# Performance work log

Hardware: AMD Instinct MI355X
Metric: run time of the kernel (lower is better)

The kernel has to match this reference:

```python
import jax, jax.numpy as jnp
import numpy as np

C = 27
SIZE = 448
PATCH = 14
G = PATCH * 4          # target_global = 56
SHN = (SIZE * SIZE) // (PATCH * PATCH)  # split_head_num = 1024
PW, GW = 0.75, 0.25    # patch_weight, global_weight
EPS = 1e-5


def setup_inputs() -> dict:
    key = jax.random.key(0)
    ks = jax.random.split(key, 9)
    s = 0.02
    return {
        "x": jax.random.normal(ks[0], (4, C, SIZE, SIZE), dtype=jnp.float32),
        "gn_w": jnp.ones((C,), jnp.float32),
        "gn_b": jnp.zeros((C,), jnp.float32),
        "q_w": jax.random.normal(ks[1], (C, C), jnp.float32) * s,
        "q_b": jax.random.normal(ks[2], (C,), jnp.float32) * s,
        "k_w": jax.random.normal(ks[3], (C, C), jnp.float32) * s,
        "k_b": jax.random.normal(ks[4], (C,), jnp.float32) * s,
        "v_w": jax.random.normal(ks[5], (C, C), jnp.float32) * s,
        "v_b": jax.random.normal(ks[6], (C,), jnp.float32) * s,
        "proj_w": jax.random.normal(ks[7], (C, C), jnp.float32) * s,
    }


def _conv1x1(w, bias, t):
    out = jnp.einsum('oc,bchw->bohw', w, t)
    return out if bias is None else out + bias[None, :, None, None]


def _bmm_attn(q, k, v, scale):
    # q,k,v: (b, d, n). w = softmax(q^T k * scale, axis=2); h = einsum over keys.
    w = jax.nn.softmax(jnp.einsum('bdn,bdm->bnm', q, k) * scale, axis=2)
    return jnp.einsum('bdj,bij->bdi', v, w)


def reference(x, gn_w, gn_b, q_w, q_b, k_w, k_b, v_w, v_b, proj_w):
    b, c, H, W = x.shape
    # GroupNorm(num_groups=1): normalize over (C,H,W) per sample
    mu = jnp.mean(x, axis=(1, 2, 3), keepdims=True)
    var = jnp.var(x, axis=(1, 2, 3), keepdims=True)
    xn = (x - mu) * jax.lax.rsqrt(var + EPS)
    xn = xn * gn_w[None, :, None, None] + gn_b[None, :, None, None]

    q = _conv1x1(q_w, q_b, xn)
    k = _conv1x1(k_w, k_b, xn)
    v = _conv1x1(v_w, v_b, xn)

    # AdaptiveAvgPool2d 448 -> 56 (exact factor 8): block mean
    f = H // G
    pool = lambda t: t.reshape(b, c, G, f, G, f).mean(axis=(3, 5))

    # patch-wise bmm attention: view (b, c*SHN, PATCH^2), attend over 196 positions
    d = c * SHN
    n = PATCH * PATCH
    qf = q.reshape(b, d, n)
    kf = k.reshape(b, d, n)
    vf = v.reshape(b, d, n)
    h_patch = _bmm_attn(qf, kf, vf, 1.0 / np.sqrt(d).astype(np.float32)).reshape(b, c, H, W)

    # global pooled bmm attention over 56*56 positions with dim c, then nearest upsample
    qg = pool(q).reshape(b, c, G * G)
    kg = pool(k).reshape(b, c, G * G)
    vg = pool(v).reshape(b, c, G * G)
    hg = _bmm_attn(qg, kg, vg, 1.0 / np.sqrt(c).astype(np.float32)).reshape(b, c, G, G)
    hg = jnp.repeat(jnp.repeat(hg, f, axis=2), f, axis=3)  # nearest upsample to (H, W)

    h_in = PW * h_patch + GW * hg
    return x + _conv1x1(proj_w, None, h_in)
```

## Files before the change

kernel.cpp:

```cpp
#include <hip/hip_runtime.h>
#include <hip/hip_bf16.h>
#include <cstdint>

namespace {
constexpr int BB = 4;
constexpr int CC = 27;
constexpr int HW = 448 * 448;
constexpr long long CHW = (long long)CC * HW;
constexpr int NP = 196;
constexpr int GG = 56 * 56;
constexpr int DTOT = CC * 1024;
constexpr float SCALE_P = 0.0060140449f;
constexpr float SCALE_G = 0.1924500897f;
constexpr float EPSV = 1e-5f;
constexpr int KCH = 512;
constexpr int NKS = DTOT / KCH;
constexpr int MPAD = 224;
constexpr int ROWB = 128;
constexpr int WFRAG = 7 * 13 * 64 * 8;
constexpr int XST = 40;
constexpr int GKC = 224;
constexpr int KST = 40;
constexpr int VST = 232;
constexpr int HST = 204;
}

typedef __attribute__((ext_vector_type(8))) short short8;
typedef __attribute__((ext_vector_type(4))) float f32x4;

__device__ __forceinline__ float bf2f(unsigned short u) {
    return __uint_as_float(((uint32_t)u) << 16);
}

__device__ __forceinline__ ushort f2bf(float f) {
    union { __hip_bfloat16 h; ushort u; } cv;
    cv.h = __float2bfloat16(f);
    return cv.u;
}

__global__ void k_fold(const float* __restrict__ pjw, const float* __restrict__ vw,
                       const float* __restrict__ vb, float* __restrict__ pvw,
                       float* __restrict__ pvb) {
    __shared__ float pj[729], vv[729], vbs[27];
    int t = threadIdx.x;
    for (int i = t; i < 729; i += 256) { pj[i] = pjw[i]; vv[i] = vw[i]; }
    if (t < 27) vbs[t] = vb[t];
    __syncthreads();
    for (int i = t; i < 729; i += 256) {
        int o = i / 27, c2 = i - (i / 27) * 27;
        float s = 0.f;
#pragma unroll
        for (int c = 0; c < 27; c++) s += pj[o * 27 + c] * vv[c * 27 + c2];
        pvw[i] = s;
    }
    if (t < 27) {
        float s = 0.f;
#pragma unroll
        for (int c = 0; c < 27; c++) s += pj[t * 27 + c] * vbs[c];
        pvb[t] = s;
    }
}

__global__ void k_gn_partial(const float* __restrict__ x, float* __restrict__ part) {
    int blk = blockIdx.x;
    int b = blk >> 10;
    int chunk = blk & 1023;
    const int CLEN = (int)(CHW / 1024);
    const float* p = x + (size_t)b * CHW + (size_t)chunk * CLEN;
    float s = 0.f, ss = 0.f;
    for (int i = threadIdx.x; i < CLEN; i += 256) {
        float v = p[i];
        s += v; ss += v * v;
    }
    for (int o = 32; o; o >>= 1) { s += __shfl_down(s, o); ss += __shfl_down(ss, o); }
    __shared__ float ls[4], lss[4];
    int wid = threadIdx.x >> 6, lane = threadIdx.x & 63;
    if (lane == 0) { ls[wid] = s; lss[wid] = ss; }
    __syncthreads();
    if (threadIdx.x == 0) {
        float S = ls[0] + ls[1] + ls[2] + ls[3];
        float SS = lss[0] + lss[1] + lss[2] + lss[3];
        part[blk * 2] = S; part[blk * 2 + 1] = SS;
    }
}

__global__ void k_gn_final(const float* __restrict__ part, float* __restrict__ stats) {
    int b = blockIdx.x;
    float s = 0.f, ss = 0.f;
    for (int i = threadIdx.x; i < 1024; i += 256) {
        s += part[(b * 1024 + i) * 2];
        ss += part[(b * 1024 + i) * 2 + 1];
    }
    for (int o = 32; o; o >>= 1) { s += __shfl_down(s, o); ss += __shfl_down(ss, o); }
    __shared__ float ls[4], lss[4];
    int wid = threadIdx.x >> 6, lane = threadIdx.x & 63;
    if (lane == 0) { ls[wid] = s; lss[wid] = ss; }
    __syncthreads();
    if (threadIdx.x == 0) {
        float S = ls[0] + ls[1] + ls[2] + ls[3];
        float SS = lss[0] + lss[1] + lss[2] + lss[3];
        float mean = S / (float)CHW;
        float var = SS / (float)CHW - mean * mean;
        stats[b * 2] = mean;
        stats[b * 2 + 1] = rsqrtf(var + EPSV);
    }
}

__global__ __launch_bounds__(256, 2)
void k_qkv_mfma(const float* __restrict__ x, const float* __restrict__ stats,
                const float* __restrict__ qw, const float* __restrict__ qb,
                const float* __restrict__ kw, const float* __restrict__ kb,
                const float* __restrict__ vw, const float* __restrict__ vb,
                const float* __restrict__ gnw, const float* __restrict__ gnb,
                __hip_bfloat16* __restrict__ qkv) {
    __shared__ ushort xs[256 * XST];
    __shared__ ushort wls[96 * XST];
    __shared__ __align__(16) float bls[96];
    __shared__ float gwls[27], gbls[27];

    int tid = threadIdx.x;
    int P0 = blockIdx.x * 256;
    int b = P0 / HW;
    int hw0 = P0 - b * HW;

    for (int i = tid; i < 96 * 32; i += 256) {
        int row = i >> 5, c = i & 31;
        float wv = 0.f;
        if (c < 27 && row < 81) {
            int t = (row >= 54) ? 2 : (row >= 27 ? 1 : 0);
            int oc = row - t * 27;
            const float* wp = (t == 0) ? qw : (t == 1) ? kw : vw;
            wv = wp[oc * 27 + c];
        }
        wls[row * XST + c] = f2bf(wv);
    }
    if (tid < 96) {
        float bv = 0.f;
        if (tid < 27) bv = qb[tid];
        else if (tid < 54) bv = kb[tid - 27];
        else if (tid < 81) bv = vb[tid - 54];
        bls[tid] = bv;
    }
    if (tid < 27) { gwls[tid] = gnw[tid]; gbls[tid] = gnb[tid]; }
    float mean = stats[b * 2], rstd = stats[b * 2 + 1];
    __syncthreads();

    {
        const float* xp = x + (size_t)b * CHW + hw0 + tid;
        ushort xv[28];
#pragma unroll
        for (int c = 0; c < 27; c++) {
            float v = (xp[(size_t)c * HW] - mean) * rstd * gwls[c] + gbls[c];
            xv[c] = f2bf(v);
        }
        xv[27] = 0;
        uint32_t* xrow = reinterpret_cast<uint32_t*>(&xs[tid * XST]);
#pragma unroll
        for (int i = 0; i < 14; i++)
            xrow[i] = (uint32_t)xv[2 * i] | ((uint32_t)xv[2 * i + 1] << 16);
        xrow[14] = 0; xrow[15] = 0;
    }
    __syncthreads();

    int w = tid >> 6, l = tid & 63;
    int lrow = l & 15, kg = l >> 4;

    short8 afr[6];
    f32x4 binit[6];
#pragma unroll
    for (int mt = 0; mt < 6; mt++) {
        afr[mt] = *reinterpret_cast<const short8*>(&wls[(mt * 16 + lrow) * XST + kg * 8]);
        binit[mt] = *reinterpret_cast<const f32x4*>(&bls[mt * 16 + kg * 4]);
    }

    f32x4 acc[4][6];
#pragma unroll
    for (int pt = 0; pt < 4; pt++) {
        const short8 bfr = *reinterpret_cast<const short8*>(
            &xs[(w * 64 + pt * 16 + lrow) * XST + kg * 8]);
#pragma unroll
        for (int mt = 0; mt < 6; mt++)
            acc[pt][mt] = __builtin_amdgcn_mfma_f32_16x16x32_bf16(afr[mt], bfr, binit[mt], 0, 0, 0);
    }

    ushort* ob = (ushort*)qkv;
#pragma unroll
    for (int pt = 0; pt < 4; pt++) {
        int hw = hw0 + w * 64 + pt * 16 + lrow;
#pragma unroll
        for (int mt = 0; mt < 6; mt++) {
#pragma unroll
            for (int r = 0; r < 4; r++) {
                int o = mt * 16 + kg * 4 + r;
                if (o < 81) {
                    int t = (o >= 54) ? 2 : (o >= 27 ? 1 : 0);
                    int oc = o - t * 27;
                    ob[((size_t)t * BB + b) * CHW + (size_t)oc * HW + hw] = f2bf(acc[pt][mt][r]);
                }
            }
        }
    }
}

__global__ void k_pool(const __hip_bfloat16* __restrict__ src, float* __restrict__ dst) {
    int idx = blockIdx.x * 256 + threadIdx.x;
    int g = idx % GG;
    int t = idx / GG;
    int c = t % 27;
    int b = t / 27;
    int gh = g / 56, gw = g - (g / 56) * 56;
    const ushort* sp = (const ushort*)src + (size_t)(b * 27 + c) * HW + (size_t)(gh * 8) * 448 + gw * 8;
    float s = 0.f;
#pragma unroll
    for (int r = 0; r < 8; r++) {
        const ushort4 a = *reinterpret_cast<const ushort4*>(sp + r * 448);
        const ushort4 d = *reinterpret_cast<const ushort4*>(sp + r * 448 + 4);
        s += bf2f(a.x) + bf2f(a.y) + bf2f(a.z) + bf2f(a.w)
           + bf2f(d.x) + bf2f(d.y) + bf2f(d.z) + bf2f(d.w);
    }
    dst[((size_t)b * GG + g) * 27 + c] = s * (1.f / 64.f);
}

__global__ __launch_bounds__(448, 1)
void k_spart_mfma(const __hip_bfloat16* __restrict__ q, const __hip_bfloat16* __restrict__ k,
                  float* __restrict__ spart) {
    __shared__ ushort lq[MPAD * 64];
    __shared__ ushort lk[MPAD * 64];
    int blk = blockIdx.x;
    int ks = blk % NKS;
    int b = blk / NKS;
    const ushort* qb_ = (const ushort*)q + (size_t)b * CHW;
    const ushort* kb_ = (const ushort*)k + (size_t)b * CHW;
    int t = threadIdx.x;
    int w = t >> 6, l = t & 63;
    int lrow = l & 15, lg = l >> 4;
    int sr = t & 15;
    int sn8 = t >> 4;

    f32x4 acc[2][13];
#pragma unroll
    for (int i = 0; i < 2; i++)
#pragma unroll
        for (int ct = 0; ct < 13; ct++) acc[i][ct] = (f32x4){0.f, 0.f, 0.f, 0.f};

    int d0 = ks * KCH;
    for (int step = 0; step < KCH / 32; ++step) {
        int dbase = d0 + step * 32;
        {
            const ushort* s0 = qb_ + (size_t)(dbase + 2 * sr) * NP + sn8 * 8;
            const ushort* s1 = s0 + NP;
            ushort4 a0 = *reinterpret_cast<const ushort4*>(s0);
            ushort4 a1 = *reinterpret_cast<const ushort4*>(s0 + 4);
            ushort4 b0 = *reinterpret_cast<const ushort4*>(s1);
            ushort4 b1 = *reinterpret_cast<const ushort4*>(s1 + 4);
            ushort ra[8] = {a0.x, a0.y, a0.z, a0.w, a1.x, a1.y, a1.z, a1.w};
            ushort rb[8] = {b0.x, b0.y, b0.z, b0.w, b1.x, b1.y, b1.z, b1.w};
#pragma unroll
            for (int kk = 0; kk < 8; kk++) {
                int n = sn8 * 8 + kk;
                uint32_t val = (uint32_t)ra[kk] | ((uint32_t)rb[kk] << 16);
                *reinterpret_cast<uint32_t*>(reinterpret_cast<char*>(lq) + n * ROWB +
                                             ((4 * sr) ^ (16 * (n & 7)))) = val;
            }
        }
        {
            const ushort* s0 = kb_ + (size_t)(dbase + 2 * sr) * NP + sn8 * 8;
            const ushort* s1 = s0 + NP;
            ushort4 a0 = *reinterpret_cast<const ushort4*>(s0);
            ushort4 a1 = *reinterpret_cast<const ushort4*>(s0 + 4);
            ushort4 b0 = *reinterpret_cast<const ushort4*>(s1);
            ushort4 b1 = *reinterpret_cast<const ushort4*>(s1 + 4);
            ushort ra[8] = {a0.x, a0.y, a0.z, a0.w, a1.x, a1.y, a1.z, a1.w};
            ushort rb[8] = {b0.x, b0.y, b0.z, b0.w, b1.x, b1.y, b1.z, b1.w};
#pragma unroll
            for (int kk = 0; kk < 8; kk++) {
                int m = sn8 * 8 + kk;
                uint32_t val = (uint32_t)ra[kk] | ((uint32_t)rb[kk] << 16);
                *reinterpret_cast<uint32_t*>(reinterpret_cast<char*>(lk) + m * ROWB +
                                             ((4 * sr) ^ (16 * (m & 7)))) = val;
            }
        }
        __syncthreads();
        int nA0 = (2 * w) * 16 + lrow;
        int nA1 = nA0 + 16;
        const short8 afr0 = *reinterpret_cast<const short8*>(
            reinterpret_cast<const char*>(lq) + nA0 * ROWB + 16 * (lg ^ (nA0 & 7)));
        const short8 afr1 = *reinterpret_cast<const short8*>(
            reinterpret_cast<const char*>(lq) + nA1 * ROWB + 16 * (lg ^ (nA1 & 7)));
#pragma unroll
        for (int ct = 0; ct < 13; ct++) {
            int m = ct * 16 + lrow;
            const short8 bfr = *reinterpret_cast<const short8*>(
                reinterpret_cast<const char*>(lk) + m * ROWB + 16 * (lg ^ (m & 7)));
            acc[0][ct] = __builtin_amdgcn_mfma_f32_16x16x32_bf16(afr0, bfr, acc[0][ct], 0, 0, 0);
            acc[1][ct] = __builtin_amdgcn_mfma_f32_16x16x32_bf16(afr1, bfr, acc[1][ct], 0, 0, 0);
        }
        __syncthreads();
    }
    float* sp = spart + (size_t)(b * NKS + ks) * NP * MPAD;
#pragma unroll
    for (int i = 0; i < 2; i++) {
        int rt = 2 * w + i;
#pragma unroll
        for (int r = 0; r < 4; r++) {
            int n = rt * 16 + lg * 4 + r;
            if (n < NP) {
#pragma unroll
                for (int ct = 0; ct < 13; ct++)
                    sp[(size_t)n * MPAD + ct * 16 + lrow] = acc[i][ct][r];
            }
        }
    }
}

__global__ void k_softmax(const float* __restrict__ spart, __hip_bfloat16* __restrict__ whf) {
    int blk = blockIdx.x;
    int n = blk % NP;
    int b = blk / NP;
    int m = threadIdx.x;
    float val = -1e30f;
    if (m < 196) {
        float s = 0.f;
        for (int ks = 0; ks < NKS; ks++)
            s += spart[((size_t)(b * NKS + ks) * NP + n) * MPAD + m];
        val = s * SCALE_P;
    }
    float mx = val;
    for (int o = 32; o; o >>= 1) mx = fmaxf(mx, __shfl_xor(mx, o));
    __shared__ float redm[4], reds[4];
    int wid = threadIdx.x >> 6, lane = threadIdx.x & 63;
    if (lane == 0) redm[wid] = mx;
    __syncthreads();
    mx = fmaxf(fmaxf(redm[0], redm[1]), fmaxf(redm[2], redm[3]));
    float p = (m < 196) ? __expf(val - mx) : 0.f;
    float sm = p;
    for (int o = 32; o; o >>= 1) sm += __shfl_xor(sm, o);
    if (lane == 0) reds[wid] = sm;
    __syncthreads();
    sm = reds[0] + reds[1] + reds[2] + reds[3];
    if (m < 224) {
        int ct = n >> 4, lr = n & 15;
        int step = m >> 5, kg = (m >> 3) & 3, e = m & 7;
        size_t addr = (size_t)b * WFRAG +
                      (((size_t)(step * 13 + ct) * 64 + kg * 16 + lr) << 3) + e;
        whf[addr] = __float2bfloat16((m < 196) ? p / sm : 0.f);
    }
}

__global__ __launch_bounds__(256)
void k_gattn_flash(const float* __restrict__ qg, const float* __restrict__ kg,
                   const float* __restrict__ vg, float* __restrict__ hg) {
    __shared__ __align__(16) ushort ksh[GKC * KST];
    __shared__ __align__(16) ushort vsh[32 * VST];
    __shared__ __align__(16) ushort psh[4][16 * VST];

    int blk = blockIdx.x;
    int b = blk / 49;
    int q0 = (blk % 49) * 64;
    int tid = threadIdx.x;
    int w = tid >> 6, l = tid & 63;
    int lr = l & 15, lg = l >> 4;

    for (int i = tid; i < GKC; i += 256) {
        ushort* kr = &ksh[i * KST];
        kr[27] = 0; kr[28] = 0; kr[29] = 0; kr[30] = 0; kr[31] = 0;
        vsh[27 * VST + i] = 0x3f80;
        vsh[28 * VST + i] = 0; vsh[29 * VST + i] = 0;
        vsh[30 * VST + i] = 0; vsh[31 * VST + i] = 0;
    }

    short8 aq;
    {
        const float* qr = qg + ((size_t)b * GG + q0 + w * 16 + lr) * 27;
#pragma unroll
        for (int j = 0; j < 8; j++) {
            int c = 8 * lg + j;
            aq[j] = (c < 27) ? (short)f2bf(qr[c]) : (short)0;
        }
    }

    f32x4 acc_h0 = {0.f, 0.f, 0.f, 0.f};
    f32x4 acc_h1 = {0.f, 0.f, 0.f, 0.f};
    ushort* myps = &psh[w][0];
    const float* kgb = kg + (size_t)b * GG * 27;
    const float* vgb = vg + (size_t)b * GG * 27;

    for (int ch = 0; ch < 14; ch++) {
        __syncthreads();
        int base = ch * GKC * 27;
        for (int idx = tid; idx < GKC * 27; idx += 256) {
            int kk = idx / 27, c = idx - (idx / 27) * 27;
            ksh[kk * KST + c] = f2bf(kgb[base + idx]);
            vsh[c * VST + kk] = f2bf(vgb[base + idx]);
        }
        __syncthreads();

        f32x4 s[14];
#pragma unroll
        for (int ct = 0; ct < 14; ct++) {
            const short8 bk = *reinterpret_cast<const short8*>(
                &ksh[(ct * 16 + lr) * KST + 8 * lg]);
            s[ct] = __builtin_amdgcn_mfma_f32_16x16x32_bf16(
                aq, bk, (f32x4){0.f, 0.f, 0.f, 0.f}, 0, 0, 0);
        }
#pragma unroll
        for (int ct = 0; ct < 14; ct++) {
#pragma unroll
            for (int r = 0; r < 4; r++) {
                float p = __expf(s[ct][r] * SCALE_G);
                myps[(4 * lg + r) * VST + ct * 16 + lr] = f2bf(p);
            }
        }
#pragma unroll
        for (int kstep = 0; kstep < 7; kstep++) {
            const short8 ap = *reinterpret_cast<const short8*>(
                &myps[lr * VST + kstep * 32 + 8 * lg]);
            const short8 bv0 = *reinterpret_cast<const short8*>(
                &vsh[lr * VST + kstep * 32 + 8 * lg]);
            const short8 bv1 = *reinterpret_cast<const short8*>(
                &vsh[(16 + lr) * VST + kstep * 32 + 8 * lg]);
            acc_h0 = __builtin_amdgcn_mfma_f32_16x16x32_bf16(ap, bv0, acc_h0, 0, 0, 0);
            acc_h1 = __builtin_amdgcn_mfma_f32_16x16x32_bf16(ap, bv1, acc_h1, 0, 0, 0);
        }
    }

#pragma unroll
    for (int r = 0; r < 4; r++) {
        float lsum = __shfl(acc_h1[r], (l & 48) | 11, 64);
        float inv = 1.f / lsum;
        int q = q0 + w * 16 + 4 * lg + r;
        float* hr = hg + ((size_t)b * GG + q) * 27;
        hr[lr] = acc_h0[r] * inv;
        if (lr < 11) hr[16 + lr] = acc_h1[r] * inv;
    }
}

__global__ __launch_bounds__(256)
void k_hp_fused(const __hip_bfloat16* __restrict__ v, const __hip_bfloat16* __restrict__ whf,
                const float* __restrict__ x, const float* __restrict__ hg,
                float* __restrict__ out) {
    __shared__ __align__(16) ushort hbuf[64 * HST];
    int nper = gridDim.x >> 3;
    int bid = blockIdx.x;
    int blk = (bid & 7) * nper + (bid >> 3);
    int b = blk / 432;
    int grp = blk % 432;
    int tid = threadIdx.x;
    int w = tid >> 6, l = tid & 63;
    int ar = l & 15;
    int kg = l >> 4;
    int D0 = (grp * 4 + w) * 16;

    int c = grp >> 4;
    int pix0 = (grp & 15) * 64 * NP;
    const float* xb = x + (size_t)b * CHW + (size_t)c * HW + pix0;
    float4 xpre[12];
#pragma unroll
    for (int it = 0; it < 12; ++it)
        xpre[it] = *reinterpret_cast<const float4*>(&xb[(tid + it * 256) * 4]);

    const ushort* vb = (const ushort*)v + (size_t)b * CHW;
    const ushort* wf = (const ushort*)whf + (size_t)b * WFRAG;

    const ushort* arow = vb + (size_t)(D0 + ar) * NP;
    short8 av[7];
#pragma unroll
    for (int step = 0; step < 7; ++step) {
        int joff = step * 32 + kg * 8;
        ushort4 alo = *reinterpret_cast<const ushort4*>(arow + joff);
        ushort4 ahi = *reinterpret_cast<const ushort4*>(arow + joff + 4);
        av[step][0] = alo.x; av[step][1] = alo.y; av[step][2] = alo.z; av[step][3] = alo.w;
        av[step][4] = ahi.x; av[step][5] = ahi.y; av[step][6] = ahi.z; av[step][7] = ahi.w;
    }

    f32x4 acc[13];
#pragma unroll
    for (int ct = 0; ct < 13; ct++) acc[ct] = (f32x4){0.f, 0.f, 0.f, 0.f};

#pragma unroll
    for (int step = 0; step < 7; ++step) {
        short8 bv[13];
#pragma unroll
        for (int ct = 0; ct < 13; ct++)
            bv[ct] = *reinterpret_cast<const short8*>(
                wf + (((size_t)(step * 13 + ct) * 64 + l) << 3));
#pragma unroll
        for (int ct = 0; ct < 13; ct++)
            acc[ct] = __builtin_amdgcn_mfma_f32_16x16x32_bf16(av[step], bv[ct], acc[ct], 0, 0, 0);
    }

#pragma unroll
    for (int ct = 0; ct < 13; ct++) {
        int i = ct * 16 + ar;
        if (i < NP) {
#pragma unroll
            for (int r = 0; r < 4; r++)
                hbuf[(w * 16 + kg * 4 + r) * HST + i] = f2bf(acc[ct][r]);
        }
    }
    __syncthreads();

    float* ob = out + (size_t)b * CHW + (size_t)c * HW + pix0;
    const float* hgb = hg + (size_t)b * GG * 27;
#pragma unroll
    for (int it = 0; it < 12; ++it) {
        int idx4 = tid + it * 256;
        int j = idx4 * 4;
        int sl = j / NP;
        int i = j - sl * NP;
        ushort4 hv = *reinterpret_cast<const ushort4*>(&hbuf[sl * HST + i]);
        int pix = pix0 + j;
        int h = pix / 448;
        int w2 = pix - h * 448;
        int g = (h >> 3) * 56 + (w2 >> 3);
        float hgs = 0.25f * hgb[g * 27 + c];
        float4 xv = xpre[it];
        float4 ov;
        ov.x = xv.x + 0.75f * bf2f(hv.x) + hgs;
        ov.y = xv.y + 0.75f * bf2f(hv.y) + hgs;
        ov.z = xv.z + 0.75f * bf2f(hv.z) + hgs;
        ov.w = xv.w + 0.75f * bf2f(hv.w) + hgs;
        *reinterpret_cast<float4*>(&ob[j]) = ov;
    }
    if (tid < 64) {
        int idx4 = 3072 + tid;
        int j = idx4 * 4;
        int sl = j / NP;
        int i = j - sl * NP;
        ushort4 hv = *reinterpret_cast<const ushort4*>(&hbuf[sl * HST + i]);
        int pix = pix0 + j;
        int h = pix / 448;
        int w2 = pix - h * 448;
        int g = (h >> 3) * 56 + (w2 >> 3);
        float hgs = 0.25f * hgb[g * 27 + c];
        float4 xv = *reinterpret_cast<const float4*>(&xb[j]);
        float4 ov;
        ov.x = xv.x + 0.75f * bf2f(hv.x) + hgs;
        ov.y = xv.y + 0.75f * bf2f(hv.y) + hgs;
        ov.z = xv.z + 0.75f * bf2f(hv.z) + hgs;
        ov.w = xv.w + 0.75f * bf2f(hv.w) + hgs;
        *reinterpret_cast<float4*>(&ob[j]) = ov;
    }
}

extern "C" void kernel_launch(void* const* d_in, const int* in_sizes, int n_in,
                              void* d_out, int out_size, void* d_ws, size_t ws_size,
                              hipStream_t stream) {
    const float* x    = (const float*)d_in[0];
    const float* gnw  = (const float*)d_in[1];
    const float* gnb  = (const float*)d_in[2];
    const float* qw   = (const float*)d_in[3];
    const float* qb   = (const float*)d_in[4];
    const float* kw   = (const float*)d_in[5];
    const float* kb   = (const float*)d_in[6];
    const float* vw   = (const float*)d_in[7];
    const float* vb   = (const float*)d_in[8];
    const float* pjw  = (const float*)d_in[9];
    float* out = (float*)d_out;

    char* ws = (char*)d_ws;
    size_t off = 0;
    auto alloc = [&](size_t bytes) { void* p = ws + off; off += (bytes + 255) & ~(size_t)255; return p; };
    __hip_bfloat16* qkvbuf = (__hip_bfloat16*)alloc((size_t)3 * BB * CHW * 2 + 64);
    __hip_bfloat16* qbf = qkvbuf;
    __hip_bfloat16* kbf = qkvbuf + (size_t)BB * CHW;
    __hip_bfloat16* vbf = qkvbuf + (size_t)2 * BB * CHW;
    float* spart = (float*)alloc((size_t)BB * NKS * NP * MPAD * 4);
    __hip_bfloat16* wHat = (__hip_bfloat16*)alloc((size_t)BB * WFRAG * 2);
    float* qg    = (float*)alloc((size_t)BB * GG * 27 * 4);
    float* kg    = (float*)alloc((size_t)BB * GG * 27 * 4);
    float* vg    = (float*)alloc((size_t)BB * GG * 27 * 4);
    float* hg    = (float*)alloc((size_t)BB * GG * 27 * 4);
    float* part  = (float*)alloc((size_t)BB * 1024 * 2 * 4);
    float* stats = (float*)alloc((size_t)BB * 2 * 4);
    float* pvw   = (float*)alloc(729 * 4);
    float* pvb   = (float*)alloc(27 * 4);

    (void)hipMemsetAsync((char*)qkvbuf + (size_t)3 * BB * CHW * 2, 0, 64, stream);
    k_fold<<<1, 256, 0, stream>>>(pjw, vw, vb, pvw, pvb);
    k_gn_partial<<<BB * 1024, 256, 0, stream>>>(x, part);
    k_gn_final<<<BB, 256, 0, stream>>>(part, stats);
    k_qkv_mfma<<<(BB * HW) / 256, 256, 0, stream>>>(x, stats, qw, qb, kw, kb, pvw, pvb,
                                                    gnw, gnb, qkvbuf);
    k_pool<<<(BB * 27 * GG) / 256, 256, 0, stream>>>(qbf, qg);
    k_pool<<<(BB * 27 * GG) / 256, 256, 0, stream>>>(kbf, kg);
    k_pool<<<(BB * 27 * GG) / 256, 256, 0, stream>>>(vbf, vg);
    k_spart_mfma<<<BB * NKS, 448, 0, stream>>>(qbf, kbf, spart);
    k_softmax<<<BB * NP, 256, 0, stream>>>(spart, wHat);
    k_gattn_flash<<<BB * 49, 256, 0, stream>>>(qg, kg, vg, hg);
    k_hp_fused<<<BB * 432, 256, 0, stream>>>(vbf, wHat, x, hg, out);
}
```

Measured before the change: 282.1 us.

## Split global attention over key chunks with a separate reduction kernel

The pooled global attention kernel now splits its 14 key chunks across 7 blocks per query tile, so the grid grows from 196 to 1372 blocks. Each block writes unnormalised partial numerators and the row-sum column to a scratch buffer, reusing the spart buffer once softmax has consumed it. A new reduce kernel sums the partials and divides by the summed denominator. The aim is to fill the many CUs that the small grid left idle. In exchange it adds an extra launch and a round trip of partial results through global memory, and it relies on the softmax not subtracting a per-chunk max, so the partial sums can simply be added.

Result: faster. 256.1 us (-9.2%).

```diff
diff --git a/kernel.cpp b/kernel.cpp
--- a/kernel.cpp
+++ b/kernel.cpp
@@ -20,6 +20,7 @@
 constexpr int WFRAG = 7 * 13 * 64 * 8;
 constexpr int XST = 40;
 constexpr int GKC = 224;
+constexpr int GKS = 7;
 constexpr int KST = 40;
 constexpr int VST = 232;
 constexpr int HST = 204;
@@ -349,14 +350,16 @@
 
 __global__ __launch_bounds__(256)
 void k_gattn_flash(const float* __restrict__ qg, const float* __restrict__ kg,
-                   const float* __restrict__ vg, float* __restrict__ hg) {
+                   const float* __restrict__ vg, float* __restrict__ pacc) {
     __shared__ __align__(16) ushort ksh[GKC * KST];
     __shared__ __align__(16) ushort vsh[32 * VST];
     __shared__ __align__(16) ushort psh[4][16 * VST];
 
     int blk = blockIdx.x;
-    int b = blk / 49;
-    int q0 = (blk % 49) * 64;
+    int ks = blk % GKS;
+    int t2 = blk / GKS;
+    int b = t2 / 49;
+    int q0 = (t2 % 49) * 64;
     int tid = threadIdx.x;
     int w = tid >> 6, l = tid & 63;
     int lr = l & 15, lg = l >> 4;
@@ -385,7 +388,7 @@
     const float* kgb = kg + (size_t)b * GG * 27;
     const float* vgb = vg + (size_t)b * GG * 27;
 
-    for (int ch = 0; ch < 14; ch++) {
+    for (int ch = ks * 2; ch < ks * 2 + 2; ch++) {
         __syncthreads();
         int base = ch * GKC * 27;
         for (int idx = tid; idx < GKC * 27; idx += 256) {
@@ -426,13 +429,27 @@
 
 #pragma unroll
     for (int r = 0; r < 4; r++) {
-        float lsum = __shfl(acc_h1[r], (l & 48) | 11, 64);
-        float inv = 1.f / lsum;
         int q = q0 + w * 16 + 4 * lg + r;
-        float* hr = hg + ((size_t)b * GG + q) * 27;
-        hr[lr] = acc_h0[r] * inv;
-        if (lr < 11) hr[16 + lr] = acc_h1[r] * inv;
-    }
+        float* pr = pacc + (((size_t)(b * GKS + ks) * GG + q) * 28);
+        pr[lr] = acc_h0[r];
+        if (lr < 12) pr[16 + lr] = acc_h1[r];
+    }
+}
+
+__global__ void k_gattn_reduce(const float* __restrict__ pacc, float* __restrict__ hg) {
+    int t = blockIdx.x * 256 + threadIdx.x;
+    if (t >= BB * GG * 27) return;
+    int c = t % 27;
+    int g = (t / 27) % GG;
+    int b = t / (27 * GG);
+    float a = 0.f, lsum = 0.f;
+#pragma unroll
+    for (int ks = 0; ks < GKS; ks++) {
+        const float* pr = pacc + (((size_t)(b * GKS + ks) * GG + g) * 28);
+        a += pr[c];
+        lsum += pr[27];
+    }
+    hg[((size_t)b * GG + g) * 27 + c] = a / lsum;
 }
 
 __global__ __launch_bounds__(256)
@@ -566,6 +583,7 @@
     __hip_bfloat16* kbf = qkvbuf + (size_t)BB * CHW;
     __hip_bfloat16* vbf = qkvbuf + (size_t)2 * BB * CHW;
     float* spart = (float*)alloc((size_t)BB * NKS * NP * MPAD * 4);
+    float* pacc  = spart;
     __hip_bfloat16* wHat = (__hip_bfloat16*)alloc((size_t)BB * WFRAG * 2);
     float* qg    = (float*)alloc((size_t)BB * GG * 27 * 4);
     float* kg    = (float*)alloc((size_t)BB * GG * 27 * 4);
@@ -587,6 +605,7 @@
     k_pool<<<(BB * 27 * GG) / 256, 256, 0, stream>>>(vbf, vg);
     k_spart_mfma<<<BB * NKS, 448, 0, stream>>>(qbf, kbf, spart);
     k_softmax<<<BB * NP, 256, 0, stream>>>(spart, wHat);
-    k_gattn_flash<<<BB * 49, 256, 0, stream>>>(qg, kg, vg, hg);
+    k_gattn_flash<<<BB * 49 * GKS, 256, 0, stream>>>(qg, kg, vg, pacc);
+    k_gattn_reduce<<<(BB * GG * 27 + 255) / 256, 256, 0, stream>>>(pacc, hg);
     k_hp_fused<<<BB * 432, 256, 0, stream>>>(vbf, wHat, x, hg, out);
 }
```
